# Performance work log

Measured on AMD Instinct MI355X. Metric: run time of the kernel, lower is better.

## Reference

```python
import jax, jax.numpy as jnp
import numpy as np

B, S, H, R, DEPTH = 64, 32, 1024, 256, 9  # batch, seq, hidden, GRU hidden (h//reduction), tree depth


def _gru(x, h, W_ih, W_hh, b_ih, b_hh):
    # PyTorch nn.GRUCell math
    gi = x @ W_ih.T + b_ih
    gh = h @ W_hh.T + b_hh
    i_r, i_z, i_n = jnp.split(gi, 3, axis=-1)
    h_r, h_z, h_n = jnp.split(gh, 3, axis=-1)
    r = jax.nn.sigmoid(i_r + h_r)
    z = jax.nn.sigmoid(i_z + h_z)
    n = jnp.tanh(i_n + r * h_n)
    return (1.0 - z) * n + z * h


def _forward(x, W_hidden, b_hidden, W_hb, b_hb, W_branch, b_branch, W_ih, W_hh, b_ih, b_hh, tree_depth):
    selu = jax.nn.selu
    # root: discretize(selu(hidden(selu(x)))).mean over sequence; discretize=identity (discretize kw None)
    xc = selu(selu(x) @ W_hidden.T + b_hidden).mean(axis=1)[:, None, :]  # [B,1,H]
    hc = jnp.zeros((x.shape[0], 1, W_hh.shape[1]), x.dtype)              # [B,1,R]
    depth = jnp.zeros((x.shape[0], 1, 1), x.dtype)
    for _ in range(tree_depth):  # level-synchronous expansion of the recursive generate()
        hc = _gru(xc, hc, W_ih, W_hh, b_ih, b_hh)
        xh = jnp.concatenate([xc, hc], axis=-1)                          # [B,N,H+R]
        hb = jax.nn.sigmoid(xh @ W_hb.T + b_hb)                          # [B,N,1]
        depth = depth + hb
        lr = selu(xh @ W_branch.T + b_branch)                            # [B,N,2H]
        l, r = jnp.split(lr, 2, axis=-1)
        l = xc - selu(l @ W_hidden.T + b_hidden)                          # residual left child
        r = xc - selu(r @ W_hidden.T + b_hidden)                          # residual right child
        Bn, N, Hd = xc.shape
        xc = jnp.stack([l, r], axis=2).reshape(Bn, 2 * N, Hd)
        hc = jnp.repeat(hc, 2, axis=1)
        depth = jnp.repeat(depth, 2, axis=1)
    # leaf nodes: final controller step; terminal = x (no V head), depth += has_branches
    hc = _gru(xc, hc, W_ih, W_hh, b_ih, b_hh)
    hb = jax.nn.sigmoid(jnp.concatenate([xc, hc], axis=-1) @ W_hb.T + b_hb)
    depth = depth + hb
    return jnp.concatenate([xc, depth], axis=-1)  # [B, 2**D, H+1]: leaf terminals + leaf depths


def setup_inputs() -> dict:
    key = jax.random.key(0)
    ks = jax.random.split(key, 6)
    def w(k, o, i):
        return (jax.random.normal(k, (o, i), jnp.float32) / np.sqrt(i)).astype(jnp.float32)
    return {
        'x': jax.random.normal(ks[0], (B, S, H), jnp.float32),
        'W_hidden': w(ks[1], H, H), 'b_hidden': jnp.zeros((H,), jnp.float32),
        'W_hb': w(ks[2], 1, H + R), 'b_hb': jnp.zeros((1,), jnp.float32),
        'W_branch': w(ks[3], 2 * H, H + R), 'b_branch': jnp.zeros((2 * H,), jnp.float32),
        'W_ih': w(ks[4], 3 * R, H), 'W_hh': w(ks[5], 3 * R, R),
        'b_ih': jnp.zeros((3 * R,), jnp.float32), 'b_hh': jnp.zeros((3 * R,), jnp.float32),
        'tree_depth': DEPTH,
    }


def reference(x, W_hidden, b_hidden, W_hb, b_hb, W_branch, b_branch, W_ih, W_hh, b_ih, b_hh, tree_depth):
    return _forward(x, W_hidden, b_hidden, W_hb, b_hb, W_branch, b_branch, W_ih, W_hh, b_ih, b_hh, tree_depth)
```

## Files before the change

kernel.cpp:

```cpp
#include <hip/hip_runtime.h>
#include <hip/hip_bf16.h>
#include <cstdint>
#include <cstddef>


#define SELU_L 1.0507009873554805f
#define SELU_A 1.6732632423543772f

__device__ __forceinline__ float selu_f(float x) {
    return x > 0.f ? SELU_L * x : (SELU_L * SELU_A) * (__expf(x) - 1.f);
}
__device__ __forceinline__ float sigmoid_f(float x) {
    return 1.f / (1.f + __expf(-x));
}

typedef __attribute__((ext_vector_type(8))) short s16x8;
typedef __attribute__((ext_vector_type(4))) float f32x4;

__device__ __forceinline__ void gld16(const void* g, void* l) {
    __builtin_amdgcn_global_load_lds(
        (const __attribute__((address_space(1))) uint32_t*)g,
        (__attribute__((address_space(3))) uint32_t*)l, 16, 0, 0);
}

enum { AM_PLAIN = 0, AM_CONCAT = 2 };
enum { EP_NONE = 0, EP_SELU32 = 1, EP_BRANCH = 2, EP_RESID = 3 };

template <int AMODE, int EPI>
__device__ __forceinline__ void gemm_body(
    int bm, int bn, int M, int K,
    const __hip_bfloat16* __restrict__ A, int lda,
    const __hip_bfloat16* __restrict__ A2,
    const __hip_bfloat16* __restrict__ W,
    const float* __restrict__ bias,
    void* __restrict__ Cv, int ldc,
    const __hip_bfloat16* __restrict__ P,
    float* __restrict__ C32, int ldc32,
    short* As, short* Bs)
{
    const int tid  = threadIdx.x;
    const int wave = tid >> 6;
    const int lane = tid & 63;

    const short* gA[4]; const short* gA2p[4]; const short* gB[4];
    short* dA[4]; short* dB[4];
#pragma unroll
    for (int r = 0; r < 4; ++r) {
        const int s   = r * 256 + wave * 64 + lane;
        const int row = s >> 3;
        const int pc  = s & 7;
        const int j   = (pc - (row >> 1)) & 7;
        const int ga  = min(bm + row, M - 1);
        if (AMODE == AM_CONCAT) {
            gA[r]   = (const short*)A  + (size_t)ga * 1024 + j * 8;
            gA2p[r] = (const short*)A2 + (size_t)ga * 256  + j * 8;
        } else {
            gA[r]   = (const short*)A + (size_t)ga * lda + j * 8;
            gA2p[r] = nullptr;
        }
        gB[r] = (const short*)W + (size_t)(bn + row) * K + j * 8;
        dA[r] = &As[(size_t)(r * 256 + wave * 64) * 8];
        dB[r] = &Bs[(size_t)(r * 256 + wave * 64) * 8];
    }

    const int wm = (wave >> 1) * 64, wn = (wave & 1) * 64;
    const int l16 = lane & 15, q4 = lane >> 4;
    int aoff[4], boff[4];
#pragma unroll
    for (int i = 0; i < 4; ++i) {
        int ra = wm + i * 16 + l16;
        aoff[i] = ra * 64 + (((q4 + (ra >> 1)) & 7) << 3);
        int rb = wn + i * 16 + l16;
        boff[i] = rb * 64 + (((q4 + (rb >> 1)) & 7) << 3);
    }

    f32x4 acc[4][4] = {};

    for (int k0 = 0; k0 < K; k0 += 64) {
#pragma unroll
        for (int r = 0; r < 4; ++r) {
            const short* ap;
            if (AMODE == AM_CONCAT)
                ap = (k0 < 1024) ? gA[r] + k0 : gA2p[r] + (k0 - 1024);
            else
                ap = gA[r] + k0;
            gld16(ap, dA[r]);
            gld16(gB[r] + k0, dB[r]);
        }
        __syncthreads();

#pragma unroll
        for (int h = 0; h < 2; ++h) {
            const int hx = h << 5;
            s16x8 af[4], bf[4];
#pragma unroll
            for (int i = 0; i < 4; ++i) af[i] = *(const s16x8*)&As[aoff[i] ^ hx];
#pragma unroll
            for (int i = 0; i < 4; ++i) bf[i] = *(const s16x8*)&Bs[boff[i] ^ hx];
#pragma unroll
            for (int mi = 0; mi < 4; ++mi)
#pragma unroll
                for (int ni = 0; ni < 4; ++ni)
                    acc[mi][ni] = __builtin_amdgcn_mfma_f32_16x16x32_bf16(
                        af[mi], bf[ni], acc[mi][ni], 0, 0, 0);
        }
        __syncthreads();
    }

    const int crow0 = bm + wm + q4 * 4;
    const int ccol0 = bn + wn + l16;
#pragma unroll
    for (int mi = 0; mi < 4; ++mi) {
#pragma unroll
        for (int r = 0; r < 4; ++r) {
            const int row = crow0 + mi * 16 + r;
            if (row >= M) continue;
#pragma unroll
            for (int ni = 0; ni < 4; ++ni) {
                const int col = ccol0 + ni * 16;
                float v = acc[mi][ni][r] + bias[col];
                if (EPI == EP_NONE) {
                    ((float*)Cv)[(size_t)row * ldc + col] = v;
                } else if (EPI == EP_SELU32) {
                    ((float*)Cv)[(size_t)row * ldc + col] = selu_f(v);
                } else if (EPI == EP_BRANCH) {
                    const int c = col >> 10, jj = col & 1023;
                    ((__hip_bfloat16*)Cv)[(size_t)(2 * row + c) * 1024 + jj] =
                        __float2bfloat16(selu_f(v));
                } else {
                    const float pv = __bfloat162float(P[(size_t)(row >> 1) * 1024 + col]);
                    const float o = pv - selu_f(v);
                    ((__hip_bfloat16*)Cv)[(size_t)row * 1024 + col] = __float2bfloat16(o);
                    if (C32) C32[(size_t)row * ldc32 + col] = o;
                }
            }
        }
    }
}

template <int AMODE, int EPI>
__global__ __launch_bounds__(256) void mgemm(
    int M, int N, int K,
    const __hip_bfloat16* __restrict__ A, int lda,
    const __hip_bfloat16* __restrict__ A2,
    const __hip_bfloat16* __restrict__ W,
    const float* __restrict__ bias,
    void* __restrict__ Cv, int ldc,
    const __hip_bfloat16* __restrict__ P,
    float* __restrict__ C32, int ldc32)
{
    __shared__ short As[8192];
    __shared__ short Bs[8192];
    int bxi = blockIdx.x, byi = blockIdx.y;
    {
        const int ncol = gridDim.x, nrow = gridDim.y;
        if ((nrow & 7) == 0) {
            const int lin = byi * ncol + bxi;
            const int xcd = lin & 7;
            const int t = lin >> 3;
            const int rows_per = nrow >> 3;
            bxi = t % ncol;
            byi = xcd * rows_per + t / ncol;
        }
    }
    gemm_body<AMODE, EPI>(byi * 128, bxi * 128, M, K, A, lda, A2, W, bias,
                          Cv, ldc, P, C32, ldc32, As, Bs);
}

struct GPair {
    int M0, K0; const __hip_bfloat16* A0; int lda0;
    const __hip_bfloat16* W0; const float* b0; float* C0; int ldc0;
    int M1, K1; const __hip_bfloat16* A1; int lda1;
    const __hip_bfloat16* W1; const float* b1; float* C1; int ldc1;
};
__global__ __launch_bounds__(256) void mgemm_pair(GPair g)
{
    __shared__ short As[8192];
    __shared__ short Bs[8192];
    int bxi = blockIdx.x, byi = blockIdx.y;
    if (blockIdx.z == 0) {
        const int ncol = gridDim.x, nrow = gridDim.y;
        if ((nrow & 7) == 0) {
            const int lin = byi * ncol + bxi;
            const int xcd = lin & 7;
            const int t = lin >> 3;
            const int rows_per = nrow >> 3;
            bxi = t % ncol;
            byi = xcd * rows_per + t / ncol;
        }
        gemm_body<AM_PLAIN, EP_NONE>(byi * 128, bxi * 128, g.M0, g.K0,
                                     g.A0, g.lda0, nullptr, g.W0, g.b0,
                                     g.C0, g.ldc0, nullptr, nullptr, 0, As, Bs);
    } else {
        if (byi * 128 >= g.M1) return;
        gemm_body<AM_PLAIN, EP_NONE>(byi * 128, bxi * 128, g.M1, g.K1,
                                     g.A1, g.lda1, nullptr, g.W1, g.b1,
                                     g.C1, g.ldc1, nullptr, nullptr, 0, As, Bs);
    }
}

__global__ void cvt4_k(const float* __restrict__ s0, __hip_bfloat16* __restrict__ d0, int n0,
                       const float* __restrict__ s1, __hip_bfloat16* __restrict__ d1, int n1,
                       const float* __restrict__ s2, __hip_bfloat16* __restrict__ d2, int n2,
                       const float* __restrict__ s3, __hip_bfloat16* __restrict__ d3, int n3)
{
    int i = blockIdx.x * 256 + threadIdx.x;
    if (i < n0) { d0[i] = __float2bfloat16(s0[i]); return; }
    i -= n0;
    if (i < n1) { d1[i] = __float2bfloat16(s1[i]); return; }
    i -= n1;
    if (i < n2) { d2[i] = __float2bfloat16(s2[i]); return; }
    i -= n2;
    if (i < n3) { d3[i] = __float2bfloat16(s3[i]); }
}

__global__ void selu_cvt_k(const float* __restrict__ in, __hip_bfloat16* __restrict__ out, int n)
{
    int i = blockIdx.x * 256 + threadIdx.x;
    if (i < n) out[i] = __float2bfloat16(selu_f(in[i]));
}

__global__ void mean_kernel(const float* __restrict__ T, __hip_bfloat16* __restrict__ xc)
{
    const int idx = blockIdx.x * 256 + threadIdx.x;
    const int b = idx >> 10, h = idx & 1023;
    const float* p = T + (size_t)b * 32 * 1024 + h;
    float s = 0.f;
#pragma unroll
    for (int si = 0; si < 32; ++si) s += p[si * 1024];
    xc[idx] = __float2bfloat16(s * (1.f / 32.f));
}

__global__ __launch_bounds__(256) void gateshb_kernel(
    const float* __restrict__ gi,
    const float* __restrict__ gh,
    const float* __restrict__ b_hh,
    const __hip_bfloat16* __restrict__ hold,
    __hip_bfloat16* __restrict__ hnew,
    const __hip_bfloat16* __restrict__ xc,
    const float* __restrict__ W_hb,
    const float* __restrict__ b_hb,
    const float* __restrict__ depth_old,
    float* __restrict__ depth_out, int dstride,
    int first)
{
    const int m = blockIdx.x;
    const int j = threadIdx.x;
    __shared__ float red[4];

    const float* gim = gi + (size_t)m * 768;
    const float ir = gim[j], iz = gim[256 + j], in_ = gim[512 + j];
    float hr, hz, hn, h0;
    if (first) {
        hr = b_hh[j]; hz = b_hh[256 + j]; hn = b_hh[512 + j]; h0 = 0.f;
    } else {
        const float* ghm = gh + (size_t)(m >> 1) * 768;
        hr = ghm[j]; hz = ghm[256 + j]; hn = ghm[512 + j];
        h0 = __bfloat162float(hold[(size_t)(m >> 1) * 256 + j]);
    }
    const float r = sigmoid_f(ir + hr);
    const float z = sigmoid_f(iz + hz);
    const float n = tanhf(in_ + r * hn);
    const float hv = (1.f - z) * n + z * h0;
    hnew[(size_t)m * 256 + j] = __float2bfloat16(hv);

    const __hip_bfloat16* xr = xc + (size_t)m * 1024;
    float s = hv * W_hb[1024 + j];
#pragma unroll
    for (int kk = 0; kk < 4; ++kk) {
        const int k = j + kk * 256;
        s += __bfloat162float(xr[k]) * W_hb[k];
    }
#pragma unroll
    for (int off = 32; off; off >>= 1) s += __shfl_down(s, off);
    if ((j & 63) == 0) red[j >> 6] = s;
    __syncthreads();
    if (j == 0) {
        const float tot = red[0] + red[1] + red[2] + red[3];
        const float hb = sigmoid_f(tot + b_hb[0]);
        const float d0 = first ? 0.f : depth_old[m >> 1];
        depth_out[(size_t)m * dstride] = d0 + hb;
    }
}

extern "C" void kernel_launch(void* const* d_in, const int* in_sizes, int n_in,
                              void* d_out, int out_size, void* d_ws, size_t ws_size,
                              hipStream_t stream)
{
    const float* x        = (const float*)d_in[0];
    const float* W_hidden = (const float*)d_in[1];
    const float* b_hidden = (const float*)d_in[2];
    const float* W_hb     = (const float*)d_in[3];
    const float* b_hb     = (const float*)d_in[4];
    const float* W_branch = (const float*)d_in[5];
    const float* b_branch = (const float*)d_in[6];
    const float* W_ih     = (const float*)d_in[7];
    const float* W_hh     = (const float*)d_in[8];
    const float* b_ih     = (const float*)d_in[9];
    const float* b_hh     = (const float*)d_in[10];

    char* ws = (char*)d_ws;
    size_t off = 0;
    auto alloc = [&](size_t bytes) {
        void* p = ws + off;
        off += (bytes + 255) & ~(size_t)255;
        return p;
    };
    __hip_bfloat16* Whb  = (__hip_bfloat16*)alloc(1024 * 1024 * 2);
    __hip_bfloat16* Wbb  = (__hip_bfloat16*)alloc(2048 * 1280 * 2);
    __hip_bfloat16* Wib  = (__hip_bfloat16*)alloc(768 * 1024 * 2);
    __hip_bfloat16* Whh  = (__hip_bfloat16*)alloc(768 * 256 * 2);
    __hip_bfloat16* Xs   = (__hip_bfloat16*)alloc((size_t)2048 * 1024 * 2);
    float*          GI   = (float*)alloc((size_t)32768 * 768 * 4);
    __hip_bfloat16* U    = (__hip_bfloat16*)alloc((size_t)32768 * 1024 * 2);
    __hip_bfloat16* XC0  = (__hip_bfloat16*)alloc((size_t)32768 * 1024 * 2);
    __hip_bfloat16* XC1  = (__hip_bfloat16*)alloc((size_t)32768 * 1024 * 2);
    __hip_bfloat16* HC0  = (__hip_bfloat16*)alloc((size_t)32768 * 256 * 2);
    __hip_bfloat16* HC1  = (__hip_bfloat16*)alloc((size_t)32768 * 256 * 2);
    float*          D0   = (float*)alloc(32768 * 4);
    float*          D1   = (float*)alloc(32768 * 4);
    float*          GH   = (float*)U;

    float* out = (float*)d_out;

    {
        const int n0 = 1024 * 1024, n1 = 2048 * 1280, n2 = 768 * 1024, n3 = 768 * 256;
        cvt4_k<<<(n0 + n1 + n2 + n3 + 255) / 256, 256, 0, stream>>>(
            W_hidden, Whb, n0, W_branch, Wbb, n1, W_ih, Wib, n2, W_hh, Whh, n3);
    }
    selu_cvt_k<<<(2048 * 1024 + 255) / 256, 256, 0, stream>>>(x, Xs, 2048 * 1024);

    mgemm<AM_PLAIN, EP_SELU32><<<dim3(1024 / 128, 2048 / 128), 256, 0, stream>>>(
        2048, 1024, 1024, Xs, 1024, nullptr, Whb, b_hidden, GI, 1024, nullptr, nullptr, 0);
    mean_kernel<<<(64 * 1024) / 256, 256, 0, stream>>>(GI, XC0);

    __hip_bfloat16* xc_cur = XC0; __hip_bfloat16* xc_next = XC1;
    __hip_bfloat16* hc_prev = nullptr; __hip_bfloat16* hc_new = HC0;
    float* d_prev = nullptr; float* d_next = D0;

    for (int d = 0; d < 9; ++d) {
        const int M = 64 << d;
        GPair g;
        g.M0 = M;     g.K0 = 1024; g.A0 = xc_cur;  g.lda0 = 1024;
        g.W0 = Wib;   g.b0 = b_ih; g.C0 = GI;      g.ldc0 = 768;
        g.M1 = M / 2; g.K1 = 256;  g.A1 = hc_prev; g.lda1 = 256;
        g.W1 = Whh;   g.b1 = b_hh; g.C1 = GH;      g.ldc1 = 768;
        mgemm_pair<<<dim3(768 / 128, (M + 127) / 128, d > 0 ? 2 : 1), 256, 0, stream>>>(g);

        gateshb_kernel<<<M, 256, 0, stream>>>(
            GI, (const float*)GH, b_hh, hc_prev, hc_new,
            xc_cur, W_hb, b_hb, d_prev, d_next, 1, d == 0 ? 1 : 0);
        mgemm<AM_CONCAT, EP_BRANCH><<<dim3(2048 / 128, (M + 127) / 128), 256, 0, stream>>>(
            M, 2048, 1280, xc_cur, 1024, hc_new, Wbb, b_branch, U, 1024, nullptr, nullptr, 0);
        mgemm<AM_PLAIN, EP_RESID><<<dim3(1024 / 128, (2 * M) / 128), 256, 0, stream>>>(
            2 * M, 1024, 1024, U, 1024, nullptr, Whb, b_hidden, xc_next, 1024,
            xc_cur, d == 8 ? out : nullptr, 1025);

        __hip_bfloat16* t = xc_cur; xc_cur = xc_next; xc_next = t;
        hc_prev = hc_new; hc_new = (hc_new == HC0) ? HC1 : HC0;
        d_prev = d_next;  d_next = (d_next == D0) ? D1 : D0;
    }

    {
        const int M = 32768;
        GPair g;
        g.M0 = M;     g.K0 = 1024; g.A0 = xc_cur;  g.lda0 = 1024;
        g.W0 = Wib;   g.b0 = b_ih; g.C0 = GI;      g.ldc0 = 768;
        g.M1 = M / 2; g.K1 = 256;  g.A1 = hc_prev; g.lda1 = 256;
        g.W1 = Whh;   g.b1 = b_hh; g.C1 = GH;      g.ldc1 = 768;
        mgemm_pair<<<dim3(768 / 128, M / 128, 2), 256, 0, stream>>>(g);
        gateshb_kernel<<<M, 256, 0, stream>>>(
            GI, (const float*)GH, b_hh, hc_prev, hc_new,
            xc_cur, W_hb, b_hb, d_prev, out + 1024, 1025, 0);
    }
}
```

Measured before the change: 1.505 ms.

## Add 256x256-tile 512-thread GEMM for the largest tree levels

Adds a new GEMM kernel with 256x256 output tiles, 8 waves per block and double-buffered LDS, each wave computing a 128x64 sub-tile. The new kernel is used for the branch and residual GEMMs at the two deepest levels and for the final-level input projection, where M is large. Larger tiles raise arithmetic intensity and cut redundant A/W reloads. The cost is higher register and LDS use, fewer resident blocks, and the final pair GEMM being split into two launches.

After: 1.596 ms. 1.06x slower.

```diff
diff --git a/kernel.cpp b/kernel.cpp
--- a/kernel.cpp
+++ b/kernel.cpp
@@ -197,6 +197,178 @@
                                      g.A1, g.lda1, nullptr, g.W1, g.b1,
                                      g.C1, g.ldc1, nullptr, nullptr, 0, As, Bs);
     }
+}
+
+template <int AMODE, int EPI>
+__device__ __forceinline__ void gemm256_body(
+    int bm, int bn, int M, int K,
+    const __hip_bfloat16* __restrict__ A, int lda,
+    const __hip_bfloat16* __restrict__ A2,
+    const __hip_bfloat16* __restrict__ W,
+    const float* __restrict__ bias,
+    void* __restrict__ Cv, int ldc,
+    const __hip_bfloat16* __restrict__ P,
+    float* __restrict__ C32, int ldc32,
+    short* As, short* Bs)
+{
+    const int tid  = threadIdx.x;
+    const int wave = tid >> 6;
+    const int lane = tid & 63;
+    const int wm = (wave >> 2) * 128;
+    const int wn = (wave & 3) * 64;
+    const int l16 = lane & 15, q4 = lane >> 4;
+
+    const short* gA[2]; const short* gA2p[2]; const short* gB[2];
+    int dOf[2];
+#pragma unroll
+    for (int r = 0; r < 2; ++r) {
+        const int s   = r * 512 + tid;
+        const int row = s >> 2;
+        const int pc  = s & 3;
+        const int j   = (pc - (row >> 1)) & 3;
+        const int ga  = min(bm + row, M - 1);
+        if (AMODE == AM_CONCAT) {
+            gA[r]   = (const short*)A  + (size_t)ga * 1024 + j * 8;
+            gA2p[r] = (const short*)A2 + (size_t)ga * 256  + j * 8;
+        } else {
+            gA[r]   = (const short*)A + (size_t)ga * lda + j * 8;
+            gA2p[r] = nullptr;
+        }
+        gB[r]  = (const short*)W + (size_t)(bn + row) * K + j * 8;
+        dOf[r] = (r * 512 + wave * 64) * 8;
+    }
+
+    int aof[2][4], bof[4];
+#pragma unroll
+    for (int mh = 0; mh < 2; ++mh)
+#pragma unroll
+        for (int i = 0; i < 4; ++i) {
+            const int ra = wm + mh * 64 + i * 16 + l16;
+            aof[mh][i] = ra * 32 + (((q4 + (ra >> 1)) & 3) << 3);
+        }
+#pragma unroll
+    for (int n = 0; n < 4; ++n) {
+        const int rb = wn + n * 16 + l16;
+        bof[n] = rb * 32 + (((q4 + (rb >> 1)) & 3) << 3);
+    }
+
+    f32x4 acc[8][4] = {};
+    const int NT = K >> 5;
+
+#pragma unroll
+    for (int r = 0; r < 2; ++r) gld16(gA[r], &As[dOf[r]]);
+#pragma unroll
+    for (int r = 0; r < 2; ++r) gld16(gB[r], &Bs[dOf[r]]);
+    asm volatile("s_waitcnt vmcnt(0)" ::: "memory");
+    __builtin_amdgcn_s_barrier();
+
+    for (int t = 0; t < NT; ++t) {
+        const int cur = (t & 1) << 13;
+        const int nxt = 8192 - cur;
+        const int k1  = (t + 1) << 5;
+
+        if (t + 1 < NT) {
+#pragma unroll
+            for (int r = 0; r < 2; ++r) {
+                const short* ap;
+                if (AMODE == AM_CONCAT)
+                    ap = (k1 < 1024) ? gA[r] + k1 : gA2p[r] + (k1 - 1024);
+                else
+                    ap = gA[r] + k1;
+                gld16(ap, &As[nxt + dOf[r]]);
+            }
+#pragma unroll
+            for (int r = 0; r < 2; ++r) gld16(gB[r] + k1, &Bs[nxt + dOf[r]]);
+        }
+        s16x8 af[4], bf[4];
+#pragma unroll
+        for (int i = 0; i < 4; ++i) af[i] = *(const s16x8*)&As[cur + aof[0][i]];
+#pragma unroll
+        for (int n = 0; n < 4; ++n) bf[n] = *(const s16x8*)&Bs[cur + bof[n]];
+        __builtin_amdgcn_s_barrier();
+        __builtin_amdgcn_s_setprio(1);
+#pragma unroll
+        for (int mi = 0; mi < 4; ++mi)
+#pragma unroll
+            for (int n = 0; n < 4; ++n)
+                acc[mi][n] = __builtin_amdgcn_mfma_f32_16x16x32_bf16(
+                    af[mi], bf[n], acc[mi][n], 0, 0, 0);
+        __builtin_amdgcn_s_setprio(0);
+        __builtin_amdgcn_s_barrier();
+
+#pragma unroll
+        for (int i = 0; i < 4; ++i) af[i] = *(const s16x8*)&As[cur + aof[1][i]];
+        __builtin_amdgcn_s_barrier();
+        __builtin_amdgcn_s_setprio(1);
+#pragma unroll
+        for (int mi = 0; mi < 4; ++mi)
+#pragma unroll
+            for (int n = 0; n < 4; ++n)
+                acc[4 + mi][n] = __builtin_amdgcn_mfma_f32_16x16x32_bf16(
+                    af[mi], bf[n], acc[4 + mi][n], 0, 0, 0);
+        __builtin_amdgcn_s_setprio(0);
+        asm volatile("s_waitcnt vmcnt(0)" ::: "memory");
+        __builtin_amdgcn_s_barrier();
+    }
+
+    const int crow0 = bm + wm + q4 * 4;
+    const int ccol0 = bn + wn + l16;
+#pragma unroll
+    for (int m8 = 0; m8 < 8; ++m8) {
+#pragma unroll
+        for (int r = 0; r < 4; ++r) {
+            const int row = crow0 + m8 * 16 + r;
+            if (row >= M) continue;
+#pragma unroll
+            for (int n4 = 0; n4 < 4; ++n4) {
+                const int col = ccol0 + n4 * 16;
+                float v = acc[m8][n4][r] + bias[col];
+                if (EPI == EP_NONE) {
+                    ((float*)Cv)[(size_t)row * ldc + col] = v;
+                } else if (EPI == EP_SELU32) {
+                    ((float*)Cv)[(size_t)row * ldc + col] = selu_f(v);
+                } else if (EPI == EP_BRANCH) {
+                    const int c = col >> 10, jj = col & 1023;
+                    ((__hip_bfloat16*)Cv)[(size_t)(2 * row + c) * 1024 + jj] =
+                        __float2bfloat16(selu_f(v));
+                } else {
+                    const float pv = __bfloat162float(P[(size_t)(row >> 1) * 1024 + col]);
+                    const float o = pv - selu_f(v);
+                    ((__hip_bfloat16*)Cv)[(size_t)row * 1024 + col] = __float2bfloat16(o);
+                    if (C32) C32[(size_t)row * ldc32 + col] = o;
+                }
+            }
+        }
+    }
+}
+
+template <int AMODE, int EPI>
+__global__ __launch_bounds__(512) void mgemm256(
+    int M, int N, int K,
+    const __hip_bfloat16* __restrict__ A, int lda,
+    const __hip_bfloat16* __restrict__ A2,
+    const __hip_bfloat16* __restrict__ W,
+    const float* __restrict__ bias,
+    void* __restrict__ Cv, int ldc,
+    const __hip_bfloat16* __restrict__ P,
+    float* __restrict__ C32, int ldc32)
+{
+    __shared__ short As[16384];
+    __shared__ short Bs[16384];
+    int bxi = blockIdx.x, byi = blockIdx.y;
+    {
+        const int ncol = gridDim.x, nrow = gridDim.y;
+        if ((nrow & 7) == 0) {
+            const int lin = byi * ncol + bxi;
+            const int xcd = lin & 7;
+            const int t = lin >> 3;
+            const int rows_per = nrow >> 3;
+            bxi = t % ncol;
+            byi = xcd * rows_per + t / ncol;
+        }
+    }
+    gemm256_body<AMODE, EPI>(byi * 256, bxi * 256, M, K, A, lda, A2, W, bias,
+                             Cv, ldc, P, C32, ldc32, As, Bs);
 }
 
 __global__ void cvt4_k(const float* __restrict__ s0, __hip_bfloat16* __restrict__ d0, int n0,
@@ -350,11 +522,22 @@
         gateshb_kernel<<<M, 256, 0, stream>>>(
             GI, (const float*)GH, b_hh, hc_prev, hc_new,
             xc_cur, W_hb, b_hb, d_prev, d_next, 1, d == 0 ? 1 : 0);
-        mgemm<AM_CONCAT, EP_BRANCH><<<dim3(2048 / 128, (M + 127) / 128), 256, 0, stream>>>(
-            M, 2048, 1280, xc_cur, 1024, hc_new, Wbb, b_branch, U, 1024, nullptr, nullptr, 0);
-        mgemm<AM_PLAIN, EP_RESID><<<dim3(1024 / 128, (2 * M) / 128), 256, 0, stream>>>(
-            2 * M, 1024, 1024, U, 1024, nullptr, Whb, b_hidden, xc_next, 1024,
-            xc_cur, d == 8 ? out : nullptr, 1025);
+
+        if (d >= 7) {
+            mgemm256<AM_CONCAT, EP_BRANCH><<<dim3(2048 / 256, M / 256), 512, 0, stream>>>(
+                M, 2048, 1280, xc_cur, 1024, hc_new, Wbb, b_branch, U, 1024,
+                nullptr, nullptr, 0);
+            mgemm256<AM_PLAIN, EP_RESID><<<dim3(1024 / 256, (2 * M) / 256), 512, 0, stream>>>(
+                2 * M, 1024, 1024, U, 1024, nullptr, Whb, b_hidden, xc_next, 1024,
+                xc_cur, d == 8 ? out : nullptr, 1025);
+        } else {
+            mgemm<AM_CONCAT, EP_BRANCH><<<dim3(2048 / 128, (M + 127) / 128), 256, 0, stream>>>(
+                M, 2048, 1280, xc_cur, 1024, hc_new, Wbb, b_branch, U, 1024,
+                nullptr, nullptr, 0);
+            mgemm<AM_PLAIN, EP_RESID><<<dim3(1024 / 128, (2 * M) / 128), 256, 0, stream>>>(
+                2 * M, 1024, 1024, U, 1024, nullptr, Whb, b_hidden, xc_next, 1024,
+                xc_cur, d == 8 ? out : nullptr, 1025);
+        }
 
         __hip_bfloat16* t = xc_cur; xc_cur = xc_next; xc_next = t;
         hc_prev = hc_new; hc_new = (hc_new == HC0) ? HC1 : HC0;
@@ -363,12 +546,12 @@
 
     {
         const int M = 32768;
-        GPair g;
-        g.M0 = M;     g.K0 = 1024; g.A0 = xc_cur;  g.lda0 = 1024;
-        g.W0 = Wib;   g.b0 = b_ih; g.C0 = GI;      g.ldc0 = 768;
-        g.M1 = M / 2; g.K1 = 256;  g.A1 = hc_prev; g.lda1 = 256;
-        g.W1 = Whh;   g.b1 = b_hh; g.C1 = GH;      g.ldc1 = 768;
-        mgemm_pair<<<dim3(768 / 128, M / 128, 2), 256, 0, stream>>>(g);
+        mgemm256<AM_PLAIN, EP_NONE><<<dim3(768 / 256, M / 256), 512, 0, stream>>>(
+            M, 768, 1024, xc_cur, 1024, nullptr, Wib, b_ih, GI, 768,
+            nullptr, nullptr, 0);
+        mgemm<AM_PLAIN, EP_NONE><<<dim3(768 / 128, (M / 2) / 128), 256, 0, stream>>>(
+            M / 2, 768, 256, hc_prev, 256, nullptr, Whh, b_hh, (void*)GH, 768,
+            nullptr, nullptr, 0);
         gateshb_kernel<<<M, 256, 0, stream>>>(
             GI, (const float*)GH, b_hh, hc_prev, hc_new,
             xc_cur, W_hb, b_hb, d_prev, out + 1024, 1025, 0);
```
